# Performance work log

Measured on AMD Instinct MI355X. Metric: run time of the kernel, lower is better.

## Reference

```python
import jax, jax.numpy as jnp
import numpy as np

B, S, D_IN, D, H = 2, 2048, 1024, 1024, 16
HD = D // H

def setup_inputs() -> dict:
    key = jax.random.key(0)
    k1, k2, k3 = jax.random.split(key, 3)
    # xavier_uniform-style scale for weights
    lim_qkv = float(np.sqrt(6.0 / (D_IN + 3 * D)))
    lim_o = float(np.sqrt(6.0 / (D + D)))
    return {
        "x": jax.random.normal(k1, (B, S, D_IN), dtype=jnp.float32),
        "w_qkv": jax.random.uniform(k2, (3 * D, D_IN), dtype=jnp.float32, minval=-lim_qkv, maxval=lim_qkv),
        "b_qkv": jnp.zeros((3 * D,), dtype=jnp.float32),
        "w_o": jax.random.uniform(k3, (D, D), dtype=jnp.float32, minval=-lim_o, maxval=lim_o),
        "b_o": jnp.zeros((D,), dtype=jnp.float32),
    }

def reference(x, w_qkv, b_qkv, w_o, b_o):
    b, s, _ = x.shape
    # QKV projection: [B,S,3D]
    qkv = jnp.einsum("bsd,ed->bse", x, w_qkv) + b_qkv
    # [B,S,H,3*HD] -> [B,H,S,3*HD]
    qkv = qkv.reshape(b, s, H, 3 * HD).transpose(0, 2, 1, 3)
    q, k, v = jnp.split(qkv, 3, axis=-1)  # each [B,H,S,HD]
    scale = 1.0 / jnp.sqrt(jnp.asarray(HD, dtype=q.dtype))
    logits = jnp.einsum("bhqd,bhkd->bhqk", q, k) * scale  # [B,H,S,S]
    attn = jax.nn.softmax(logits, axis=-1)
    vals = jnp.einsum("bhqk,bhkd->bhqd", attn, v)  # [B,H,S,HD]
    vals = vals.transpose(0, 2, 1, 3).reshape(b, s, D)
    return jnp.einsum("bsd,ed->bse", vals, w_o) + b_o
```

## Files before the change

### kernel.cpp

```cpp
#include <hip/hip_runtime.h>
#include <hip/hip_bf16.h>
#include <math.h>

#define BATCH 2
#define SLEN  2048
#define DIN   1024
#define DMODEL 1024
#define NHEAD 16
#define HD    64
#define E3    3072

typedef unsigned short us;
typedef _Float16 f16;
typedef __attribute__((ext_vector_type(8))) _Float16 f16x8;
typedef __attribute__((ext_vector_type(2))) _Float16 f16x2;
typedef __attribute__((ext_vector_type(8))) unsigned short us8;
typedef __attribute__((ext_vector_type(4))) unsigned short us4;
typedef __attribute__((ext_vector_type(4))) float f32x4;
typedef __attribute__((ext_vector_type(16))) float f32x16;
typedef __attribute__((ext_vector_type(4))) unsigned int u32x4;

#define QSCALE 0.18033688011112042f

__device__ __forceinline__ us f16bits(float x) {
    const f16 h = (f16)x;
    return __builtin_bit_cast(us, h);
}

__device__ __forceinline__ unsigned int pkrtz(float a, float b) {
    return __builtin_bit_cast(unsigned int, __builtin_amdgcn_cvt_pkrtz(a, b));
}

__device__ __forceinline__ void plswap(unsigned int& a, unsigned int& b) {
    asm volatile("v_permlane32_swap_b32 %0, %1" : "+v"(a), "+v"(b));
}

#define GLL16(g, l)                                                                     \
    __builtin_amdgcn_global_load_lds((const __attribute__((address_space(1))) unsigned int*)(g), \
                                     (__attribute__((address_space(3))) unsigned int*)(l), 16, 0, 0)

__global__ __launch_bounds__(256) void cvt3_f16(
    const float* __restrict__ x, us* __restrict__ ox, int nx,
    const float* __restrict__ wq, us* __restrict__ owq, int nq,
    const float* __restrict__ wo, us* __restrict__ owo)
{
    int i = (blockIdx.x * 256 + threadIdx.x) * 8;
    const float* s;
    us* o;
    if (i < nx)           { s = x;  o = ox; }
    else if (i < nx + nq) { s = wq; o = owq; i -= nx; }
    else                  { s = wo; o = owo; i -= nx + nq; }
    const float4 f0 = *(const float4*)&s[i];
    const float4 f1 = *(const float4*)&s[i + 4];
    const float v[8] = {f0.x, f0.y, f0.z, f0.w, f1.x, f1.y, f1.z, f1.w};
    us8 h;
#pragma unroll
    for (int j = 0; j < 8; ++j) h[j] = f16bits(v[j]);
    *(us8*)&o[i] = h;
}

template <bool QKV_OUT>
__global__ __launch_bounds__(256) void gemm_f16(
    const us* __restrict__ Am, const us* __restrict__ Bm,
    const float* __restrict__ bias, void* __restrict__ Cout,
    int M, int N, int K)
{
    __shared__ __align__(16) us As[128 * 32];
    __shared__ __align__(16) us Bs[128 * 32];

    const int t    = threadIdx.x;
    const int lane = t & 63;
    const int w    = t >> 6;
    const int ml   = lane & 15;
    const int quad = lane >> 4;
    const int wm   = w >> 1;
    const int wn   = w & 1;

    const int m0 = blockIdx.y * 128;
    const int n0 = blockIdx.x * 128;

    const int srow = (lane >> 2);
    const int scol = (lane & 3) * 8;

    const us* pA = Am + (size_t)(m0 + w * 32 + srow) * K + scol;
    const us* pB = Bm + (size_t)(n0 + w * 32 + srow) * K + scol;
    const size_t rstep = (size_t)16 * K;

    us* lA0 = &As[(w * 32) * 32];
    us* lA1 = &As[(w * 32 + 16) * 32];
    us* lB0 = &Bs[(w * 32) * 32];
    us* lB1 = &Bs[(w * 32 + 16) * 32];

    f32x4 acc[4][4];
#pragma unroll
    for (int i = 0; i < 4; ++i)
#pragma unroll
        for (int j = 0; j < 4; ++j) {
            acc[i][j][0] = 0.f; acc[i][j][1] = 0.f; acc[i][j][2] = 0.f; acc[i][j][3] = 0.f;
        }

    for (int k0 = 0; k0 < K; k0 += 32) {
        __syncthreads();
        GLL16(pA + k0, lA0); GLL16(pA + k0 + rstep, lA1);
        GLL16(pB + k0, lB0); GLL16(pB + k0 + rstep, lB1);
        __syncthreads();

        f16x8 a[4];
#pragma unroll
        for (int i = 0; i < 4; ++i)
            a[i] = __builtin_bit_cast(f16x8, *(const us8*)&As[(wm * 64 + i * 16 + ml) * 32 + quad * 8]);
#pragma unroll
        for (int j = 0; j < 4; ++j) {
            const f16x8 b = __builtin_bit_cast(f16x8, *(const us8*)&Bs[(wn * 64 + j * 16 + ml) * 32 + quad * 8]);
#pragma unroll
            for (int i = 0; i < 4; ++i)
                acc[i][j] = __builtin_amdgcn_mfma_f32_16x16x32_f16(a[i], b, acc[i][j], 0, 0, 0);
        }
    }

    float bj[4], cs[4];
#pragma unroll
    for (int j = 0; j < 4; ++j) {
        const int col = n0 + wn * 64 + j * 16 + ml;
        bj[j] = bias[col];
        cs[j] = (QKV_OUT && (col % 192) < 64) ? QSCALE : 1.0f;
    }

#pragma unroll
    for (int i = 0; i < 4; ++i) {
#pragma unroll
        for (int r = 0; r < 4; ++r) {
            const size_t rowoff = (size_t)(m0 + wm * 64 + i * 16 + quad * 4 + r) * N;
#pragma unroll
            for (int j = 0; j < 4; ++j) {
                const int col = n0 + wn * 64 + j * 16 + ml;
                const float v = (acc[i][j][r] + bj[j]) * cs[j];
                if (QKV_OUT) ((us*)Cout)[rowoff + col] = f16bits(v);
                else         ((float*)Cout)[rowoff + col] = v;
            }
        }
    }
}

#define ABQ 128
#define ACH 64
#define NCH (SLEN / ACH)
#define NCH2 (NCH / 2)
#define LQA 72
#define OSTR 68

__global__ __launch_bounds__(512, 4) void attn_mfma(
    const us* __restrict__ qkvh, us* __restrict__ vals)
{
    __shared__ __align__(16) us smem[27648];
    us* const Qs = smem;
    us* const Ks = smem + 9216;
    us* const Vt = smem + 18432;

    const int t    = threadIdx.x;
    const int lane = t & 63;
    const int w    = t >> 6;
    const int sp   = w >> 2;
    const int wq4  = w & 3;
    const int t2   = t & 255;
    const int m32  = lane & 31;
    const int half = lane >> 5;

    const int bh = blockIdx.y;
    const int b  = bh >> 4;
    const int h  = bh & 15;
    const int q0 = blockIdx.x * ABQ;

    const size_t base = (size_t)b * SLEN * E3;
    const int qoff = h * 192;

    {
        const int row = t >> 2;
        const int c0q = (t & 3) * 16;
        const us* g = &qkvh[base + (size_t)(q0 + row) * E3 + qoff + c0q];
        *(us8*)&Qs[row * LQA + c0q]     = *(const us8*)g;
        *(us8*)&Qs[row * LQA + c0q + 8] = *(const us8*)(g + 8);
    }
    __syncthreads();

    f16x8 aq[4];
#pragma unroll
    for (int s = 0; s < 4; ++s)
        aq[s] = __builtin_bit_cast(f16x8, *(const us8*)&Qs[(wq4 * 32 + m32) * LQA + half * 8 + 16 * s]);

    const int krA = t2 >> 2;
    const int ksA = (t2 & 3) * 16;
    const int k2  = t2 & 31;
    const int d0v = (t2 >> 5) * 8;

    us* const myK = Ks + sp * 4608;
    us* const myV = Vt + sp * 4608;
    const int cg0 = sp * NCH2;

    us8 kk0, kk1, vv0, vv1;
    {
        const us* gK = &qkvh[base + (size_t)(cg0 * ACH + krA) * E3 + qoff + 64 + ksA];
        kk0 = *(const us8*)gK; kk1 = *(const us8*)(gK + 8);
        const us* gV = &qkvh[base + (size_t)(cg0 * ACH + 2 * k2) * E3 + qoff + 128 + d0v];
        vv0 = *(const us8*)gV; vv1 = *(const us8*)(gV + E3);
    }

    f32x16 O[2];
#pragma unroll
    for (int dt = 0; dt < 2; ++dt)
#pragma unroll
        for (int r = 0; r < 16; ++r) O[dt][r] = 0.f;
    float lpart = 0.f;

    for (int c = 0; c < NCH2; ++c) {
        __syncthreads();
        *(us8*)&myK[krA * LQA + ksA]     = kk0;
        *(us8*)&myK[krA * LQA + ksA + 8] = kk1;
#pragma unroll
        for (int j = 0; j < 8; ++j) {
            const unsigned int pv = (unsigned int)vv0[j] | ((unsigned int)vv1[j] << 16);
            *(unsigned int*)&myV[(d0v + j) * LQA + 2 * k2] = pv;
        }
        __syncthreads();
        if (c + 1 < NCH2) {
            const int cg = cg0 + c + 1;
            const us* gK = &qkvh[base + (size_t)(cg * ACH + krA) * E3 + qoff + 64 + ksA];
            kk0 = *(const us8*)gK; kk1 = *(const us8*)(gK + 8);
            const us* gV = &qkvh[base + (size_t)(cg * ACH + 2 * k2) * E3 + qoff + 128 + d0v];
            vv0 = *(const us8*)gV; vv1 = *(const us8*)(gV + E3);
        }

        f16x8 pf[4];
#pragma unroll
        for (int kt = 0; kt < 2; ++kt) {
            f32x16 z;
#pragma unroll
            for (int r = 0; r < 16; ++r) z[r] = 0.f;
#pragma unroll
            for (int s = 0; s < 4; ++s) {
                const f16x8 ak = __builtin_bit_cast(f16x8, *(const us8*)&myK[(kt * 32 + m32) * LQA + half * 8 + 16 * s]);
                z = __builtin_amdgcn_mfma_f32_32x32x16_f16(ak, aq[s], z, 0, 0, 0);
            }
            float p[16];
#pragma unroll
            for (int r = 0; r < 16; ++r) {
                p[r] = __builtin_amdgcn_exp2f(z[r]);
                lpart += p[r];
            }
            unsigned int a0 = pkrtz(p[0],  p[1]),  a1 = pkrtz(p[2],  p[3]);
            unsigned int b0 = pkrtz(p[4],  p[5]),  b1 = pkrtz(p[6],  p[7]);
            plswap(a0, b0); plswap(a1, b1);
            pf[2 * kt] = __builtin_bit_cast(f16x8, (u32x4){a0, a1, b0, b1});
            unsigned int e0 = pkrtz(p[8],  p[9]),  e1 = pkrtz(p[10], p[11]);
            unsigned int f0 = pkrtz(p[12], p[13]), f1 = pkrtz(p[14], p[15]);
            plswap(e0, f0); plswap(e1, f1);
            pf[2 * kt + 1] = __builtin_bit_cast(f16x8, (u32x4){e0, e1, f0, f1});
        }

#pragma unroll
        for (int dt = 0; dt < 2; ++dt) {
#pragma unroll
            for (int s = 0; s < 4; ++s) {
                const f16x8 av = __builtin_bit_cast(f16x8, *(const us8*)&myV[(dt * 32 + m32) * LQA + half * 8 + 16 * s]);
                O[dt] = __builtin_amdgcn_mfma_f32_32x32x16_f16(av, pf[s], O[dt], 0, 0, 0);
            }
        }
    }

    const float l = lpart + __shfl_xor(lpart, 32);
    const int ql = wq4 * 32 + m32;

    __syncthreads();
    float* const Osc = (float*)(smem + 9216);
    float* const lsc = Osc + ABQ * OSTR;

    if (sp == 1) {
#pragma unroll
        for (int dt = 0; dt < 2; ++dt) {
#pragma unroll
            for (int g = 0; g < 4; ++g) {
                const f32x4 o4 = {O[dt][g * 4], O[dt][g * 4 + 1], O[dt][g * 4 + 2], O[dt][g * 4 + 3]};
                *(f32x4*)&Osc[ql * OSTR + dt * 32 + 8 * g + 4 * half] = o4;
            }
        }
        if (half == 0) lsc[ql] = l;
    }
    __syncthreads();
    if (sp == 0) {
        const float rl = 1.0f / (l + lsc[ql]);
        const int sq = q0 + ql;
        const size_t rowbase = (size_t)(b * SLEN + sq) * DMODEL + h * HD;
#pragma unroll
        for (int dt = 0; dt < 2; ++dt) {
#pragma unroll
            for (int g = 0; g < 4; ++g) {
                const f32x4 part = *(const f32x4*)&Osc[ql * OSTR + dt * 32 + 8 * g + 4 * half];
                us4 o4;
#pragma unroll
                for (int r2 = 0; r2 < 4; ++r2)
                    o4[r2] = f16bits((O[dt][g * 4 + r2] + part[r2]) * rl);
                *(us4*)&vals[rowbase + dt * 32 + 8 * g + 4 * half] = o4;
            }
        }
    }
}

extern "C" void kernel_launch(void* const* d_in, const int* in_sizes, int n_in,
                              void* d_out, int out_size, void* d_ws, size_t ws_size,
                              hipStream_t stream) {
    const float* x     = (const float*)d_in[0];
    const float* w_qkv = (const float*)d_in[1];
    const float* b_qkv = (const float*)d_in[2];
    const float* w_o   = (const float*)d_in[3];
    const float* b_o   = (const float*)d_in[4];
    float* out = (float*)d_out;

    const int M   = BATCH * SLEN;
    const int XN  = M * DIN;
    const int WQN = E3 * DIN;
    const int WON = DMODEL * DMODEL;
    const size_t QKVN = (size_t)BATCH * SLEN * E3;

    us* qkvh = (us*)d_ws;
    us* xh   = qkvh + QKVN;
    us* wq   = xh + XN;
    us* wo   = wq + WQN;

    cvt3_f16<<<dim3((XN + WQN + WON) / 2048), 256, 0, stream>>>(
        x, xh, XN, w_qkv, wq, WQN, w_o, wo);

    gemm_f16<true><<<dim3(E3 / 128, M / 128), 256, 0, stream>>>(
        xh, wq, b_qkv, qkvh, M, E3, DIN);

    us* vals = xh;
    attn_mfma<<<dim3(SLEN / ABQ, BATCH * NHEAD), 512, 0, stream>>>(qkvh, vals);

    gemm_f16<false><<<dim3(DMODEL / 128, M / 128), 256, 0, stream>>>(
        vals, wo, b_o, out, M, DMODEL, DMODEL);
}
```

Before: 190.3 us.

## Add 256x256-tile pipelined f16 GEMM for QKV projection

```diff
diff --git a/kernel.cpp b/kernel.cpp
--- a/kernel.cpp
+++ b/kernel.cpp
@@ -13,7 +13,6 @@
 typedef unsigned short us;
 typedef _Float16 f16;
 typedef __attribute__((ext_vector_type(8))) _Float16 f16x8;
-typedef __attribute__((ext_vector_type(2))) _Float16 f16x2;
 typedef __attribute__((ext_vector_type(8))) unsigned short us8;
 typedef __attribute__((ext_vector_type(4))) unsigned short us4;
 typedef __attribute__((ext_vector_type(4))) float f32x4;
@@ -33,6 +32,10 @@
 
 __device__ __forceinline__ void plswap(unsigned int& a, unsigned int& b) {
     asm volatile("v_permlane32_swap_b32 %0, %1" : "+v"(a), "+v"(b));
+}
+
+__device__ __forceinline__ void barrier_raw() {
+    asm volatile("s_barrier" ::: "memory");
 }
 
 #define GLL16(g, l)                                                                     \
@@ -59,6 +62,133 @@
     *(us8*)&o[i] = h;
 }
 
+#define GBK 64
+#define GNT (DIN / GBK)
+
+template <bool QKV_OUT>
+__global__ __launch_bounds__(512, 2) void gemm256_f16(
+    const us* __restrict__ Am, const us* __restrict__ Bm,
+    const float* __restrict__ bias, void* __restrict__ Cout,
+    int M, int N, int K)
+{
+    __shared__ __align__(16) us lds[65536];
+    us* const ldsA = lds;
+    us* const ldsB = lds + 32768;
+
+    const int t    = threadIdx.x;
+    const int lane = t & 63;
+    const int w    = t >> 6;
+    const int ml   = lane & 15;
+    const int quad = lane >> 4;
+    const int msk  = ml & 7;
+
+    const int nbx = N >> 8;
+    const int nwg = (M >> 8) * nbx;
+    int wg = blockIdx.y * nbx + blockIdx.x;
+    wg = (wg & 7) * (nwg >> 3) + (wg >> 3);
+    const int m0 = (wg / nbx) * 256;
+    const int n0 = (wg % nbx) * 256;
+
+    const int r8  = lane >> 3;
+    const int xsw = ((lane & 7) ^ r8) * 8;
+    const us* pA0 = Am + (size_t)(m0 + w * 16 + r8) * K + xsw;
+    const us* pA1 = pA0 + (size_t)8 * K;
+    const us* pB0 = Bm + (size_t)(n0 + w * 16 + r8) * K + xsw;
+    const us* pB1 = pB0 + (size_t)8 * K;
+    const int sdo = w * 1024;
+
+#define STG_A(d, half, kk) do { \
+    GLL16(pA0 + (size_t)(half) * 128 * K + (kk), &ldsA[(d) * 16384 + (half) * 8192 + sdo]); \
+    GLL16(pA1 + (size_t)(half) * 128 * K + (kk), &ldsA[(d) * 16384 + (half) * 8192 + sdo + 512]); } while (0)
+#define STG_B(d, half, kk) do { \
+    GLL16(pB0 + (size_t)(half) * 128 * K + (kk), &ldsB[(d) * 16384 + (half) * 8192 + sdo]); \
+    GLL16(pB1 + (size_t)(half) * 128 * K + (kk), &ldsB[(d) * 16384 + (half) * 8192 + sdo + 512]); } while (0)
+
+#define LDA(d, mi, ks) __builtin_bit_cast(f16x8, *(const us8*)&ldsA[(d) * 16384 + ((mi) * 16 + ml) * 64 + (((quad ^ msk) ^ ((ks) << 2)) * 8)])
+#define LDB(d, nj, ks) __builtin_bit_cast(f16x8, *(const us8*)&ldsB[(d) * 16384 + (w * 32 + (nj) * 16 + ml) * 64 + (((quad ^ msk) ^ ((ks) << 2)) * 8)])
+
+    f32x4 acc[16][2];
+#pragma unroll
+    for (int i = 0; i < 16; ++i)
+#pragma unroll
+        for (int j = 0; j < 2; ++j) {
+            acc[i][j][0] = 0.f; acc[i][j][1] = 0.f; acc[i][j][2] = 0.f; acc[i][j][3] = 0.f;
+        }
+
+#define PHASE(q) do { \
+    f16x8 aa[4][2]; \
+    _Pragma("unroll") for (int mi2 = 0; mi2 < 4; ++mi2) { \
+        aa[mi2][0] = LDA(d, (q) * 4 + mi2, 0); \
+        aa[mi2][1] = LDA(d, (q) * 4 + mi2, 1); } \
+    __builtin_amdgcn_s_setprio(1); \
+    _Pragma("unroll") for (int ks = 0; ks < 2; ++ks) \
+    _Pragma("unroll") for (int nj = 0; nj < 2; ++nj) \
+    _Pragma("unroll") for (int mi2 = 0; mi2 < 4; ++mi2) \
+        acc[(q) * 4 + mi2][nj] = __builtin_amdgcn_mfma_f32_16x16x32_f16(aa[mi2][ks], bf[ks][nj], acc[(q) * 4 + mi2][nj], 0, 0, 0); \
+    __builtin_amdgcn_s_setprio(0); \
+} while (0)
+
+    STG_A(0, 0, 0); STG_A(0, 1, 0); STG_B(0, 0, 0); STG_B(0, 1, 0);
+    STG_A(1, 0, GBK);
+    asm volatile("s_waitcnt vmcnt(2)" ::: "memory");
+    barrier_raw();
+
+    for (int tt = 0; tt < GNT; ++tt) {
+        const int d = tt & 1, e = d ^ 1;
+        const int kn = (tt + 1) * GBK;
+
+        if (tt + 1 < GNT) { STG_A(e, 1, kn); STG_B(e, 0, kn); }
+        f16x8 bf[2][2];
+#pragma unroll
+        for (int ks = 0; ks < 2; ++ks)
+#pragma unroll
+            for (int nj = 0; nj < 2; ++nj)
+                bf[ks][nj] = LDB(d, nj, ks);
+        PHASE(0);
+        barrier_raw();
+
+        if (tt + 1 < GNT) STG_B(e, 1, kn);
+        PHASE(1);
+        barrier_raw();
+
+        if (tt + 2 < GNT) STG_A(d, 0, kn + GBK);
+        PHASE(2);
+        barrier_raw();
+
+        PHASE(3);
+        if (tt + 2 < GNT)      { asm volatile("s_waitcnt vmcnt(2)" ::: "memory"); }
+        else if (tt + 1 < GNT) { asm volatile("s_waitcnt vmcnt(0)" ::: "memory"); }
+        barrier_raw();
+    }
+
+    float bj[2], cs[2];
+#pragma unroll
+    for (int nj = 0; nj < 2; ++nj) {
+        const int col = n0 + w * 32 + nj * 16 + ml;
+        bj[nj] = bias[col];
+        cs[nj] = (QKV_OUT && (col % 192) < 64) ? QSCALE : 1.0f;
+    }
+#pragma unroll
+    for (int mi = 0; mi < 16; ++mi) {
+#pragma unroll
+        for (int r = 0; r < 4; ++r) {
+            const size_t rowoff = (size_t)(m0 + mi * 16 + quad * 4 + r) * N;
+#pragma unroll
+            for (int nj = 0; nj < 2; ++nj) {
+                const int col = n0 + w * 32 + nj * 16 + ml;
+                const float v = (acc[mi][nj][r] + bj[nj]) * cs[nj];
+                if (QKV_OUT) ((us*)Cout)[rowoff + col] = f16bits(v);
+                else         ((float*)Cout)[rowoff + col] = v;
+            }
+        }
+    }
+#undef PHASE
+#undef LDA
+#undef LDB
+#undef STG_A
+#undef STG_B
+}
+
 template <bool QKV_OUT>
 __global__ __launch_bounds__(256) void gemm_f16(
     const us* __restrict__ Am, const us* __restrict__ Bm,
@@ -329,7 +459,7 @@
     cvt3_f16<<<dim3((XN + WQN + WON) / 2048), 256, 0, stream>>>(
         x, xh, XN, w_qkv, wq, WQN, w_o, wo);
 
-    gemm_f16<true><<<dim3(E3 / 128, M / 128), 256, 0, stream>>>(
+    gemm256_f16<true><<<dim3(E3 / 256, M / 256), 512, 0, stream>>>(
         xh, wq, b_qkv, qkvh, M, E3, DIN);
 
     us* vals = xh;
```

Result: no change. 187.6 us (-1.4%).

## Double-buffer GEMM with swizzled LDS, XCD-aware block remap, smaller output-GEMM tile

Applied to the files above, without the earlier changes.

```diff
diff --git a/kernel.cpp b/kernel.cpp
--- a/kernel.cpp
+++ b/kernel.cpp
@@ -13,7 +13,6 @@
 typedef unsigned short us;
 typedef _Float16 f16;
 typedef __attribute__((ext_vector_type(8))) _Float16 f16x8;
-typedef __attribute__((ext_vector_type(2))) _Float16 f16x2;
 typedef __attribute__((ext_vector_type(8))) unsigned short us8;
 typedef __attribute__((ext_vector_type(4))) unsigned short us4;
 typedef __attribute__((ext_vector_type(4))) float f32x4;
@@ -33,6 +32,10 @@
 
 __device__ __forceinline__ void plswap(unsigned int& a, unsigned int& b) {
     asm volatile("v_permlane32_swap_b32 %0, %1" : "+v"(a), "+v"(b));
+}
+
+__device__ __forceinline__ void barrier_raw() {
+    asm volatile("s_barrier" ::: "memory");
 }
 
 #define GLL16(g, l)                                                                     \
@@ -59,87 +62,141 @@
     *(us8*)&o[i] = h;
 }
 
-template <bool QKV_OUT>
-__global__ __launch_bounds__(256) void gemm_f16(
+#define GBK 64
+#define GNT (DIN / GBK)
+
+template <int BN, bool QKV_OUT>
+__global__ __launch_bounds__(256) void gemm_db(
     const us* __restrict__ Am, const us* __restrict__ Bm,
     const float* __restrict__ bias, void* __restrict__ Cout,
     int M, int N, int K)
 {
-    __shared__ __align__(16) us As[128 * 32];
-    __shared__ __align__(16) us Bs[128 * 32];
+    constexpr int NJ  = BN / 32;
+    constexpr int BGL = BN / 32;
+    __shared__ __align__(16) us ldsA[2 * 128 * 64];
+    __shared__ __align__(16) us ldsB[2 * BN * 64];
 
     const int t    = threadIdx.x;
     const int lane = t & 63;
     const int w    = t >> 6;
     const int ml   = lane & 15;
     const int quad = lane >> 4;
+    const int msk  = ml & 7;
     const int wm   = w >> 1;
     const int wn   = w & 1;
 
-    const int m0 = blockIdx.y * 128;
-    const int n0 = blockIdx.x * 128;
-
-    const int srow = (lane >> 2);
-    const int scol = (lane & 3) * 8;
-
-    const us* pA = Am + (size_t)(m0 + w * 32 + srow) * K + scol;
-    const us* pB = Bm + (size_t)(n0 + w * 32 + srow) * K + scol;
-    const size_t rstep = (size_t)16 * K;
-
-    us* lA0 = &As[(w * 32) * 32];
-    us* lA1 = &As[(w * 32 + 16) * 32];
-    us* lB0 = &Bs[(w * 32) * 32];
-    us* lB1 = &Bs[(w * 32 + 16) * 32];
-
-    f32x4 acc[4][4];
+    const int nbx = N / BN;
+    const int nwg = (M >> 7) * nbx;
+    int wg = blockIdx.y * nbx + blockIdx.x;
+    wg = (wg & 7) * (nwg >> 3) + (wg >> 3);
+    const int m0 = (wg / nbx) * 128;
+    const int n0 = (wg % nbx) * BN;
+
+    const int r8  = lane >> 3;
+    const int xsw = ((lane & 7) ^ r8) * 8;
+    const us* pA = Am + (size_t)(m0 + w * 32 + r8) * K + xsw;
+    const int brow = (BN == 128) ? w * 32 : w * 16;
+    const us* pB = Bm + (size_t)(n0 + brow + r8) * K + xsw;
+
+#define STG_A(d, kk) do { _Pragma("unroll") for (int g = 0; g < 4; ++g) \
+    GLL16(pA + (size_t)(8 * g) * K + (kk), &ldsA[(d) * 8192 + w * 2048 + g * 512]); } while (0)
+#define STG_B(d, kk) do { _Pragma("unroll") for (int g = 0; g < BGL; ++g) \
+    GLL16(pB + (size_t)(8 * g) * K + (kk), &ldsB[(d) * (BN * 64) + brow * 64 + g * 512]); } while (0)
+
+#define LDA(d, mi, ks) __builtin_bit_cast(f16x8, *(const us8*)&ldsA[(d) * 8192 + (wm * 64 + (mi) * 16 + ml) * 64 + (((quad ^ msk) ^ ((ks) << 2)) * 8)])
+#define LDB(d, nj, ks) __builtin_bit_cast(f16x8, *(const us8*)&ldsB[(d) * (BN * 64) + (wn * (BN / 2) + (nj) * 16 + ml) * 64 + (((quad ^ msk) ^ ((ks) << 2)) * 8)])
+
+#define WAIT_BGL() do { if constexpr (BN == 128) asm volatile("s_waitcnt vmcnt(4)" ::: "memory"); \
+                        else                     asm volatile("s_waitcnt vmcnt(2)" ::: "memory"); } while (0)
+
+    f32x4 acc[4][NJ];
 #pragma unroll
     for (int i = 0; i < 4; ++i)
 #pragma unroll
-        for (int j = 0; j < 4; ++j) {
+        for (int j = 0; j < NJ; ++j) {
             acc[i][j][0] = 0.f; acc[i][j][1] = 0.f; acc[i][j][2] = 0.f; acc[i][j][3] = 0.f;
         }
 
-    for (int k0 = 0; k0 < K; k0 += 32) {
-        __syncthreads();
-        GLL16(pA + k0, lA0); GLL16(pA + k0 + rstep, lA1);
-        GLL16(pB + k0, lB0); GLL16(pB + k0 + rstep, lB1);
-        __syncthreads();
-
-        f16x8 a[4];
-#pragma unroll
-        for (int i = 0; i < 4; ++i)
-            a[i] = __builtin_bit_cast(f16x8, *(const us8*)&As[(wm * 64 + i * 16 + ml) * 32 + quad * 8]);
-#pragma unroll
-        for (int j = 0; j < 4; ++j) {
-            const f16x8 b = __builtin_bit_cast(f16x8, *(const us8*)&Bs[(wn * 64 + j * 16 + ml) * 32 + quad * 8]);
-#pragma unroll
-            for (int i = 0; i < 4; ++i)
-                acc[i][j] = __builtin_amdgcn_mfma_f32_16x16x32_f16(a[i], b, acc[i][j], 0, 0, 0);
-        }
-    }
-
-    float bj[4], cs[4];
-#pragma unroll
-    for (int j = 0; j < 4; ++j) {
-        const int col = n0 + wn * 64 + j * 16 + ml;
-        bj[j] = bias[col];
-        cs[j] = (QKV_OUT && (col % 192) < 64) ? QSCALE : 1.0f;
-    }
-
-#pragma unroll
-    for (int i = 0; i < 4; ++i) {
+    STG_A(0, 0); STG_B(0, 0);
+    STG_B(1, GBK);
+    WAIT_BGL();
+    barrier_raw();
+
+    for (int tt = 0; tt < GNT; ++tt) {
+        const int d = tt & 1, e = d ^ 1;
+
+        if (tt + 1 < GNT) STG_A(e, (tt + 1) * GBK);
+        f16x8 bf[2][NJ];
+#pragma unroll
+        for (int ks = 0; ks < 2; ++ks)
+#pragma unroll
+            for (int nj = 0; nj < NJ; ++nj)
+                bf[ks][nj] = LDB(d, nj, ks);
+        f16x8 a0[2][2];
+#pragma unroll
+        for (int mi = 0; mi < 2; ++mi) {
+            a0[mi][0] = LDA(d, mi, 0);
+            a0[mi][1] = LDA(d, mi, 1);
+        }
+        __builtin_amdgcn_s_setprio(1);
+#pragma unroll
+        for (int ks = 0; ks < 2; ++ks)
+#pragma unroll
+            for (int nj = 0; nj < NJ; ++nj)
+#pragma unroll
+                for (int mi = 0; mi < 2; ++mi)
+                    acc[mi][nj] = __builtin_amdgcn_mfma_f32_16x16x32_f16(a0[mi][ks], bf[ks][nj], acc[mi][nj], 0, 0, 0);
+        __builtin_amdgcn_s_setprio(0);
+        barrier_raw();
+
+        if (tt + 2 < GNT) STG_B(d, (tt + 2) * GBK);
+        f16x8 a1[2][2];
+#pragma unroll
+        for (int mi = 0; mi < 2; ++mi) {
+            a1[mi][0] = LDA(d, mi + 2, 0);
+            a1[mi][1] = LDA(d, mi + 2, 1);
+        }
+        __builtin_amdgcn_s_setprio(1);
+#pragma unroll
+        for (int ks = 0; ks < 2; ++ks)
+#pragma unroll
+            for (int nj = 0; nj < NJ; ++nj)
+#pragma unroll
+                for (int mi = 0; mi < 2; ++mi)
+                    acc[mi + 2][nj] = __builtin_amdgcn_mfma_f32_16x16x32_f16(a1[mi][ks], bf[ks][nj], acc[mi + 2][nj], 0, 0, 0);
+        __builtin_amdgcn_s_setprio(0);
+
+        if (tt + 2 < GNT)      WAIT_BGL();
+        else if (tt + 1 < GNT) asm volatile("s_waitcnt vmcnt(0)" ::: "memory");
+        barrier_raw();
+    }
+
+    float bj[NJ], cs[NJ];
+#pragma unroll
+    for (int nj = 0; nj < NJ; ++nj) {
+        const int col = n0 + wn * (BN / 2) + nj * 16 + ml;
+        bj[nj] = bias[col];
+        cs[nj] = (QKV_OUT && (col % 192) < 64) ? QSCALE : 1.0f;
+    }
+#pragma unroll
+    for (int mi = 0; mi < 4; ++mi) {
 #pragma unroll
         for (int r = 0; r < 4; ++r) {
-            const size_t rowoff = (size_t)(m0 + wm * 64 + i * 16 + quad * 4 + r) * N;
-#pragma unroll
-            for (int j = 0; j < 4; ++j) {
-                const int col = n0 + wn * 64 + j * 16 + ml;
-                const float v = (acc[i][j][r] + bj[j]) * cs[j];
+            const size_t rowoff = (size_t)(m0 + wm * 64 + mi * 16 + quad * 4 + r) * N;
+#pragma unroll
+            for (int nj = 0; nj < NJ; ++nj) {
+                const int col = n0 + wn * (BN / 2) + nj * 16 + ml;
+                const float v = (acc[mi][nj][r] + bj[nj]) * cs[nj];
                 if (QKV_OUT) ((us*)Cout)[rowoff + col] = f16bits(v);
                 else         ((float*)Cout)[rowoff + col] = v;
             }
         }
     }
+#undef STG_A
+#undef STG_B
+#undef LDA
+#undef LDB
+#undef WAIT_BGL
 }
 
 #define ABQ 128
@@ -166,10 +223,12 @@
     const int m32  = lane & 31;
     const int half = lane >> 5;
 
-    const int bh = blockIdx.y;
-    const int b  = bh >> 4;
-    const int h  = bh & 15;
-    const int q0 = blockIdx.x * ABQ;
+    const int wg  = blockIdx.x;
+    const int s9  = wg >> 3;
+    const int bh  = ((s9 >> 4) << 3) | (wg & 7);
+    const int b   = bh >> 4;
+    const int h   = bh & 15;
+    const int q0  = (s9 & 15) * ABQ;
 
     const size_t base = (size_t)b * SLEN * E3;
     const int qoff = h * 192;
@@ -329,12 +388,12 @@
     cvt3_f16<<<dim3((XN + WQN + WON) / 2048), 256, 0, stream>>>(
         x, xh, XN, w_qkv, wq, WQN, w_o, wo);
 
-    gemm_f16<true><<<dim3(E3 / 128, M / 128), 256, 0, stream>>>(
+    gemm_db<128, true><<<dim3(E3 / 128, M / 128), 256, 0, stream>>>(
         xh, wq, b_qkv, qkvh, M, E3, DIN);
 
     us* vals = xh;
-    attn_mfma<<<dim3(SLEN / ABQ, BATCH * NHEAD), 512, 0, stream>>>(qkvh, vals);
-
-    gemm_f16<false><<<dim3(DMODEL / 128, M / 128), 256, 0, stream>>>(
+    attn_mfma<<<dim3((SLEN / ABQ) * BATCH * NHEAD), 512, 0, stream>>>(qkvh, vals);
+
+    gemm_db<64, false><<<dim3(DMODEL / 64, M / 128), 256, 0, stream>>>(
         vals, wo, b_o, out, M, DMODEL, DMODEL);
 }
```

Result: faster. 185.5 us (-2.5%).
